# Optimization experiments

Hardware: AMD Instinct MI355X
Metric: run time of the kernel (lower is better)

## Reference

```python
import jax, jax.numpy as jnp
import numpy as np


def setup_inputs() -> dict:
    key = jax.random.key(0)
    k_idx, k_val = jax.random.split(key)
    XSIZE = 128
    N = 500000
    B = 16
    indices = jax.random.randint(k_idx, (N, 3), 0, XSIZE, dtype=jnp.int32)
    values = jax.random.normal(k_val, (B, N), dtype=jnp.float32)
    return {"indices": indices, "values": values, "xsize": XSIZE}


def reference(indices, values, xsize):
    # densitySmoothnessVolume: scatter-add values into a (B, X, X, X) grid,
    # then TV and MSE smoothness losses over 3-axis finite differences.
    B = values.shape[0]
    X = xsize
    # flat voxel index (z, y, x) -> z*X*X + y*X + x ; shared across batch
    flat = (indices[:, 0].astype(jnp.int32) * X + indices[:, 1]) * X + indices[:, 2]
    grid = jnp.zeros((B, X * X * X), dtype=values.dtype)
    grid = grid.at[:, flat].add(values)  # scatter-add, duplicate indices accumulate
    grid = grid.reshape(B, X, X, X)

    d1 = grid[:, 1:, :, :] - grid[:, :-1, :, :]
    d2 = grid[:, :, 1:, :] - grid[:, :, :-1, :]
    d3 = grid[:, :, :, 1:] - grid[:, :, :, :-1]

    axes = (1, 2, 3)
    # total variation loss, normalized by number of voxels X^3
    num_pixels = jnp.asarray(X * X * X, dtype=values.dtype)
    tv = (jnp.sum(jnp.abs(d1), axis=axes)
          + jnp.sum(jnp.abs(d2), axis=axes)
          + jnp.sum(jnp.abs(d3), axis=axes)) / num_pixels

    # MSE smoothness loss; normalizer replicates TF code exactly:
    # 2 * prod(shape[1:3]) - shape[1] - shape[2] = 2*X^2 - 2*X
    num_pixel_pairs = jnp.asarray(2 * X * X - 2 * X, dtype=values.dtype)
    mse = (jnp.sum(jnp.square(d1), axis=axes)
           + jnp.sum(jnp.square(d2), axis=axes)
           + jnp.sum(jnp.square(d3), axis=axes)) / num_pixel_pairs

    return jnp.stack([tv, mse])  # [2, B]
```

## Files before the change

kernel.cpp:

```cpp
#include <hip/hip_runtime.h>

#define XS 128
#define PLANE (XS * XS)
#define X3 (XS * XS * XS)
#define ZC 4
#define TPB 1024
#define SLOTS 4
#define QPT 4
#define CAP 8192

__device__ __forceinline__ void bar_lgkm() {
    __builtin_amdgcn_sched_barrier(0);
    asm volatile("s_waitcnt lgkmcnt(0)" ::: "memory");
    __builtin_amdgcn_s_barrier();
    __builtin_amdgcn_sched_barrier(0);
}

__global__ __launch_bounds__(256) void init_kernel(
    int* __restrict__ cursor, float* __restrict__ out, int osz)
{
    const int t = threadIdx.x;
    if (t < XS) cursor[t] = 0;
    if (t < osz) out[t] = 0.f;
}

__global__ __launch_bounds__(256) void reorder_kernel(
    const int* __restrict__ idx, int* __restrict__ cursor,
    int2* __restrict__ list, int N)
{
    __shared__ int lh[XS], lbase[XS];
    const int c0 = blockIdx.x * 1024;
    const int t = threadIdx.x;
    int z[4], key[4], nn[4];
    int cntm = 0;

    for (int i = t; i < XS; i += 256) lh[i] = 0;

    if (c0 + 1024 <= N) {
        const int4* p = (const int4*)(idx + (size_t)c0 * 3);
        int4 A = p[3 * t], B4 = p[3 * t + 1], C = p[3 * t + 2];
        const int nb = c0 + 4 * t;
        z[0] = A.x;  key[0] = (A.y << 7) | A.z;   nn[0] = nb;
        z[1] = A.w;  key[1] = (B4.x << 7) | B4.y; nn[1] = nb + 1;
        z[2] = B4.z; key[2] = (B4.w << 7) | C.x;  nn[2] = nb + 2;
        z[3] = C.y;  key[3] = (C.z << 7) | C.w;   nn[3] = nb + 3;
        cntm = 4;
    } else {
        #pragma unroll
        for (int i = 0; i < 4; ++i) {
            const int n = c0 + 4 * t + i;
            if (n < N) {
                z[cntm]   = idx[3 * n];
                key[cntm] = (idx[3 * n + 1] << 7) | idx[3 * n + 2];
                nn[cntm]  = n;
                ++cntm;
            }
        }
    }
    __syncthreads();
    #pragma unroll
    for (int i = 0; i < 4; ++i)
        if (i < cntm) atomicAdd(&lh[z[i]], 1);
    __syncthreads();
    for (int i = t; i < XS; i += 256) {
        lbase[i] = lh[i] ? atomicAdd(&cursor[i], lh[i]) : 0;
        lh[i] = 0;
    }
    __syncthreads();
    #pragma unroll
    for (int i = 0; i < 4; ++i)
        if (i < cntm) {
            const int r = atomicAdd(&lh[z[i]], 1);
            list[(size_t)z[i] * CAP + lbase[z[i]] + r] = make_int2(nn[i], key[i]);
        }
}

__global__ __launch_bounds__(TPB, 8) void fused_kernel(
    const int2* __restrict__ list, const int* __restrict__ cnt,
    const float* __restrict__ vals, float* __restrict__ out,
    int N, int Btot)
{
    __shared__ float buf[PLANE];
    __shared__ float rtv[TPB / 64], rms[TPB / 64];

    const int b   = blockIdx.x;
    const int z0  = blockIdx.y * ZC;
    const int tid = threadIdx.x;
    const float* vb = vals + (size_t)b * N;
    const int pmax = (z0 + ZC < XS) ? (z0 + ZC) : (XS - 1);

    int pos[SLOTS]; float val[SLOTS];
    int pc = 0, ps0 = 0;

    auto prefetch = [&](int zp) {
        ps0 = zp * CAP; pc = cnt[zp];
        int2 e[SLOTS];
        #pragma unroll
        for (int i = 0; i < SLOTS; ++i)
            e[i] = list[(size_t)ps0 + tid + i * TPB];
        #pragma unroll
        for (int i = 0; i < SLOTS; ++i) {
            const unsigned nx = (unsigned)e[i].x < (unsigned)N ? e[i].x : 0u;
            pos[i] = e[i].y & (PLANE - 1);
            val[i] = vb[nx];
        }
    };
    auto scatter = [&]() {
        #pragma unroll
        for (int i = 0; i < SLOTS; ++i) {
            const float v = (tid + i * TPB < pc) ? val[i] : 0.f;
            atomicAdd(&buf[pos[i]], v);
        }
        for (int e = SLOTS * TPB + tid; e < pc; e += TPB) {
            const int2 en = list[(size_t)ps0 + e];
            atomicAdd(&buf[en.y], vb[en.x]);
        }
    };

    prefetch(z0);
    #pragma unroll
    for (int i = 0; i < QPT; ++i)
        ((float4*)buf)[tid + i * TPB] = make_float4(0.f, 0.f, 0.f, 0.f);
    bar_lgkm();
    scatter();
    prefetch(z0 + 1);
    bar_lgkm();

    float4 prev[QPT];
    float tv = 0.f, ms = 0.f;

    for (int p = z0; p <= pmax; ++p) {
        float4 a[QPT];
        #pragma unroll
        for (int i = 0; i < QPT; ++i)
            a[i] = ((const float4*)buf)[tid + i * TPB];

        if (p > z0) {
            #pragma unroll
            for (int i = 0; i < QPT; ++i) {
                float d;
                d = a[i].x - prev[i].x; tv += fabsf(d); ms += d * d;
                d = a[i].y - prev[i].y; tv += fabsf(d); ms += d * d;
                d = a[i].z - prev[i].z; tv += fabsf(d); ms += d * d;
                d = a[i].w - prev[i].w; tv += fabsf(d); ms += d * d;
            }
        }
        if (p < z0 + ZC) {
            #pragma unroll
            for (int i = 0; i < QPT; ++i) {
                const int q = tid + i * TPB;
                const int qx = q & 31, y = q >> 5;
                float d;
                d = a[i].y - a[i].x; tv += fabsf(d); ms += d * d;
                d = a[i].z - a[i].y; tv += fabsf(d); ms += d * d;
                d = a[i].w - a[i].z; tv += fabsf(d); ms += d * d;
                if (qx < 31) {
                    d = buf[4 * q + 4] - a[i].w; tv += fabsf(d); ms += d * d;
                }
                if (y < XS - 1) {
                    const float4 u = ((const float4*)buf)[q + 32];
                    d = u.x - a[i].x; tv += fabsf(d); ms += d * d;
                    d = u.y - a[i].y; tv += fabsf(d); ms += d * d;
                    d = u.z - a[i].z; tv += fabsf(d); ms += d * d;
                    d = u.w - a[i].w; tv += fabsf(d); ms += d * d;
                }
            }
        }
        #pragma unroll
        for (int i = 0; i < QPT; ++i) prev[i] = a[i];

        if (p < pmax) {
            bar_lgkm();
            #pragma unroll
            for (int i = 0; i < QPT; ++i)
                ((float4*)buf)[tid + i * TPB] = make_float4(0.f, 0.f, 0.f, 0.f);
            bar_lgkm();
            scatter();
            if (p + 2 <= pmax) prefetch(p + 2);
            bar_lgkm();
        }
    }

    for (int o = 32; o > 0; o >>= 1) {
        tv += __shfl_down(tv, o); ms += __shfl_down(ms, o);
    }
    if ((tid & 63) == 0) { rtv[tid >> 6] = tv; rms[tid >> 6] = ms; }
    __syncthreads();
    if (tid == 0) {
        float t = 0.f, m = 0.f;
        #pragma unroll
        for (int w = 0; w < TPB / 64; ++w) { t += rtv[w]; m += rms[w]; }
        atomicAdd(out + b,        t * (1.0f / (float)X3));
        atomicAdd(out + Btot + b, m * (1.0f / (float)(2 * XS * XS - 2 * XS)));
    }
}

extern "C" void kernel_launch(void* const* d_in, const int* in_sizes, int n_in,
                              void* d_out, int out_size, void* d_ws, size_t ws_size,
                              hipStream_t stream)
{
    const int*   indices = (const int*)d_in[0];
    const float* values  = (const float*)d_in[1];
    const int N = in_sizes[0] / 3;
    const int B = in_sizes[1] / N;
    float* out = (float*)d_out;
    char*  ws  = (char*)d_ws;

    int2* list   = (int2*)ws;
    int*  cursor = (int*)(ws + (size_t)XS * CAP * sizeof(int2));

    init_kernel<<<1, 256, 0, stream>>>(cursor, out, out_size);
    reorder_kernel<<<(N + 1023) / 1024, 256, 0, stream>>>(
        indices, cursor, list, N);
    fused_kernel<<<dim3(B, XS / ZC), TPB, 0, stream>>>(
        list, cursor, values, out, N, B);
}
```

Measured before the change: 179.9 us.

## Pre-gather batch values into z-bucketed transposed array during reorder

The reorder kernel now also copies all 16 batch values of each point into a slot-ordered array (16 floats per slot), and stores only 16-bit in-plane positions. The fused kernel then reads values by slot index instead of doing random gathers into the values tensor through stored point indices. This trades the random per-batch gather for an extra 32MB-scale write in reorder and strided reads in the fused kernel, which rely on L2 sharing across the 16 batch blocks.

New measurement: 180.1 us. About the same (+0.1%).

```diff
diff --git a/kernel.cpp b/kernel.cpp
--- a/kernel.cpp
+++ b/kernel.cpp
@@ -26,24 +26,25 @@
 
 __global__ __launch_bounds__(256) void reorder_kernel(
     const int* __restrict__ idx, int* __restrict__ cursor,
-    int2* __restrict__ list, int N)
+    const float* __restrict__ vals, float* __restrict__ pvT,
+    unsigned short* __restrict__ posArr, int N)
 {
     __shared__ int lh[XS], lbase[XS];
     const int c0 = blockIdx.x * 1024;
     const int t = threadIdx.x;
-    int z[4], key[4], nn[4];
+    int z[4], key[4];
     int cntm = 0;
+    const bool fast = (c0 + 1024 <= N);
 
     for (int i = t; i < XS; i += 256) lh[i] = 0;
 
-    if (c0 + 1024 <= N) {
+    if (fast) {
         const int4* p = (const int4*)(idx + (size_t)c0 * 3);
         int4 A = p[3 * t], B4 = p[3 * t + 1], C = p[3 * t + 2];
-        const int nb = c0 + 4 * t;
-        z[0] = A.x;  key[0] = (A.y << 7) | A.z;   nn[0] = nb;
-        z[1] = A.w;  key[1] = (B4.x << 7) | B4.y; nn[1] = nb + 1;
-        z[2] = B4.z; key[2] = (B4.w << 7) | C.x;  nn[2] = nb + 2;
-        z[3] = C.y;  key[3] = (C.z << 7) | C.w;   nn[3] = nb + 3;
+        z[0] = A.x;  key[0] = (A.y << 7) | A.z;
+        z[1] = A.w;  key[1] = (B4.x << 7) | B4.y;
+        z[2] = B4.z; key[2] = (B4.w << 7) | C.x;
+        z[3] = C.y;  key[3] = (C.z << 7) | C.w;
         cntm = 4;
     } else {
         #pragma unroll
@@ -52,7 +53,6 @@
             if (n < N) {
                 z[cntm]   = idx[3 * n];
                 key[cntm] = (idx[3 * n + 1] << 7) | idx[3 * n + 2];
-                nn[cntm]  = n;
                 ++cntm;
             }
         }
@@ -67,18 +67,46 @@
         lh[i] = 0;
     }
     __syncthreads();
+
+    int slot[4];
     #pragma unroll
     for (int i = 0; i < 4; ++i)
         if (i < cntm) {
             const int r = atomicAdd(&lh[z[i]], 1);
-            list[(size_t)z[i] * CAP + lbase[z[i]] + r] = make_int2(nn[i], key[i]);
-        }
+            slot[i] = z[i] * CAP + lbase[z[i]] + r;
+            posArr[slot[i]] = (unsigned short)key[i];
+        }
+
+    if (fast) {
+        float4 vv[16];
+        #pragma unroll
+        for (int b = 0; b < 16; ++b)
+            vv[b] = *(const float4*)(vals + (size_t)b * N + c0 + 4 * t);
+        #pragma unroll
+        for (int i = 0; i < 4; ++i) {
+            float4* dst = (float4*)(pvT + (size_t)slot[i] * 16);
+            float4 w0 = make_float4(((const float*)&vv[0])[i],  ((const float*)&vv[1])[i],
+                                    ((const float*)&vv[2])[i],  ((const float*)&vv[3])[i]);
+            float4 w1 = make_float4(((const float*)&vv[4])[i],  ((const float*)&vv[5])[i],
+                                    ((const float*)&vv[6])[i],  ((const float*)&vv[7])[i]);
+            float4 w2 = make_float4(((const float*)&vv[8])[i],  ((const float*)&vv[9])[i],
+                                    ((const float*)&vv[10])[i], ((const float*)&vv[11])[i]);
+            float4 w3 = make_float4(((const float*)&vv[12])[i], ((const float*)&vv[13])[i],
+                                    ((const float*)&vv[14])[i], ((const float*)&vv[15])[i]);
+            dst[0] = w0; dst[1] = w1; dst[2] = w2; dst[3] = w3;
+        }
+    } else {
+        for (int i = 0; i < cntm; ++i) {
+            const int n = c0 + 4 * t + i;
+            float* dst = pvT + (size_t)slot[i] * 16;
+            for (int b = 0; b < 16; ++b) dst[b] = vals[(size_t)b * N + n];
+        }
+    }
 }
 
 __global__ __launch_bounds__(TPB, 8) void fused_kernel(
-    const int2* __restrict__ list, const int* __restrict__ cnt,
-    const float* __restrict__ vals, float* __restrict__ out,
-    int N, int Btot)
+    const unsigned short* __restrict__ posArr, const int* __restrict__ cnt,
+    const float* __restrict__ pvT, float* __restrict__ out, int Btot)
 {
     __shared__ float buf[PLANE];
     __shared__ float rtv[TPB / 64], rms[TPB / 64];
@@ -86,7 +114,6 @@
     const int b   = blockIdx.x;
     const int z0  = blockIdx.y * ZC;
     const int tid = threadIdx.x;
-    const float* vb = vals + (size_t)b * N;
     const int pmax = (z0 + ZC < XS) ? (z0 + ZC) : (XS - 1);
 
     int pos[SLOTS]; float val[SLOTS];
@@ -94,15 +121,11 @@
 
     auto prefetch = [&](int zp) {
         ps0 = zp * CAP; pc = cnt[zp];
-        int2 e[SLOTS];
-        #pragma unroll
-        for (int i = 0; i < SLOTS; ++i)
-            e[i] = list[(size_t)ps0 + tid + i * TPB];
         #pragma unroll
         for (int i = 0; i < SLOTS; ++i) {
-            const unsigned nx = (unsigned)e[i].x < (unsigned)N ? e[i].x : 0u;
-            pos[i] = e[i].y & (PLANE - 1);
-            val[i] = vb[nx];
+            const int sx = ps0 + tid + i * TPB;
+            pos[i] = posArr[sx] & (PLANE - 1);
+            val[i] = pvT[(size_t)sx * 16 + b];
         }
     };
     auto scatter = [&]() {
@@ -112,8 +135,8 @@
             atomicAdd(&buf[pos[i]], v);
         }
         for (int e = SLOTS * TPB + tid; e < pc; e += TPB) {
-            const int2 en = list[(size_t)ps0 + e];
-            atomicAdd(&buf[en.y], vb[en.x]);
+            atomicAdd(&buf[posArr[ps0 + e] & (PLANE - 1)],
+                      pvT[(size_t)(ps0 + e) * 16 + b]);
         }
     };
 
@@ -206,12 +229,13 @@
     float* out = (float*)d_out;
     char*  ws  = (char*)d_ws;
 
-    int2* list   = (int2*)ws;
-    int*  cursor = (int*)(ws + (size_t)XS * CAP * sizeof(int2));
+    float* pvT = (float*)ws;
+    unsigned short* posArr = (unsigned short*)(ws + (size_t)XS * CAP * 16 * sizeof(float));
+    int* cursor = (int*)((char*)posArr + (size_t)XS * CAP * sizeof(unsigned short));
 
     init_kernel<<<1, 256, 0, stream>>>(cursor, out, out_size);
     reorder_kernel<<<(N + 1023) / 1024, 256, 0, stream>>>(
-        indices, cursor, list, N);
+        indices, cursor, values, pvT, posArr, N);
     fused_kernel<<<dim3(B, XS / ZC), TPB, 0, stream>>>(
-        list, cursor, values, out, N, B);
-}
+        posArr, cursor, pvT, out, B);
+}
```
